# Performance work log

Measured on AMD Instinct MI355X. Metric: run time of the kernel, lower is better.

## Reference

```python
import jax, jax.numpy as jnp
import numpy as np

DIM_IN = 384
DIM_V = 384
NUM_HEADS = 8
DIM_FF = 1536
B, N = 4, 2048


def setup_inputs() -> dict:
    key = jax.random.key(0)
    ks = jax.random.split(key, 7)
    s_in = 1.0 / np.sqrt(DIM_IN)
    s_v = 1.0 / np.sqrt(DIM_V)
    s_ff = 1.0 / np.sqrt(DIM_FF)
    return {
        "x": jax.random.normal(ks[0], (B, N, DIM_IN), jnp.float32),
        "y": jax.random.normal(ks[1], (B, N, DIM_IN), jnp.float32),
        "Wq": jax.random.normal(ks[2], (DIM_V, DIM_IN), jnp.float32) * s_in,
        "Wk": jax.random.normal(ks[3], (DIM_V, DIM_IN), jnp.float32) * s_in,
        "Wv": jax.random.normal(ks[4], (DIM_V, DIM_IN), jnp.float32) * s_in,
        "W1": jax.random.normal(ks[5], (DIM_FF, DIM_V), jnp.float32) * s_v,
        "W2": jax.random.normal(ks[6], (DIM_V, DIM_FF), jnp.float32) * s_ff,
    }


def reference(x, y, Wq, Wk, Wv, W1, W2):
    H = NUM_HEADS
    d = DIM_V // H  # per-head dim
    Q = jnp.einsum('bnd,vd->bnv', x, Wq)
    K = jnp.einsum('bnd,vd->bnv', y, Wk)
    V = jnp.einsum('bnd,vd->bnv', y, Wv)
    # split channels into heads: [B, H, N, d]
    def to_heads(t):
        b, n, _ = t.shape
        return t.reshape(b, n, H, d).transpose(0, 2, 1, 3)
    Qh, Kh, Vh = to_heads(Q), to_heads(K), to_heads(V)
    # NOTE: original scales by sqrt(dim_V) (full model dim), not per-head dim
    scores = jnp.einsum('bhid,bhjd->bhij', Qh, Kh) / jnp.sqrt(jnp.float32(DIM_V))
    attn = jax.nn.softmax(scores, axis=-1)  # dropout = identity in eval
    A = jnp.einsum('bhij,bhjd->bhid', attn, Vh)
    # residual per-head, then merge heads back to [B, N, dim_V]
    O = (Qh + A).transpose(0, 2, 1, 3).reshape(x.shape[0], x.shape[1], DIM_V)
    # FFN with exact-erf gelu (torch F.gelu default) and residual
    hidden = jax.nn.gelu(jnp.einsum('bnv,fv->bnf', O, W1), approximate=False)
    O = O + jnp.einsum('bnf,vf->bnv', hidden, W2)
    return O
```

## Files before the change

kernel.cpp:

```cpp
#include <hip/hip_runtime.h>
#include <stdint.h>

#define NB 4
#define NSEQ 2048
#define DIN 384
#define DV 384
#define NH 8
#define DH 48
#define DFF 1536
#define MTOT (NB*NSEQ)
#define QBLK 128

typedef __attribute__((ext_vector_type(8))) short bf16x8;
typedef __attribute__((ext_vector_type(4))) float f32x4;
typedef unsigned short u16;

#define SCALE2 0.07362222f

__device__ __forceinline__ u16 f2bf(float f) {
  unsigned u = __builtin_bit_cast(unsigned, f);
  u = (u + 0x7FFFu + ((u >> 16) & 1u)) >> 16;
  return (u16)u;
}
__device__ __forceinline__ float bf2f(u16 h) {
  unsigned u = ((unsigned)h) << 16;
  return __builtin_bit_cast(float, u);
}
__device__ __forceinline__ float ex2(float x) {
  float r; asm("v_exp_f32 %0, %1" : "=v"(r) : "v"(x)); return r;
}
__device__ __forceinline__ float frcp(float x) {
  float r; asm("v_rcp_f32 %0, %1" : "=v"(r) : "v"(x)); return r;
}

__device__ __forceinline__ void gload16(const u16* g, u16* l) {
  __builtin_amdgcn_global_load_lds(
      (const __attribute__((address_space(1))) void*)g,
      (__attribute__((address_space(3))) void*)l, 16, 0, 0);
}

__global__ __launch_bounds__(256) void convert_k(
    const float* __restrict__ xf, const float* __restrict__ yf,
    const float* __restrict__ wq, const float* __restrict__ wk,
    const float* __restrict__ wv, const float* __restrict__ w1,
    const float* __restrict__ w2,
    u16* __restrict__ xb, u16* __restrict__ yb,
    u16* __restrict__ wqb, u16* __restrict__ wkb, u16* __restrict__ wvb,
    u16* __restrict__ w1b, u16* __restrict__ w2b) {
  long i = (long)blockIdx.x * 256 + threadIdx.x;
  const float* src; u16* dst; long u = i;
  if      (u < 786432)  { src = xf; dst = xb; }
  else if (u < 1572864) { u -= 786432;  src = yf; dst = yb; }
  else if (u < 1609728) { u -= 1572864; src = wq; dst = wqb; }
  else if (u < 1646592) { u -= 1609728; src = wk; dst = wkb; }
  else if (u < 1683456) { u -= 1646592; src = wv; dst = wvb; }
  else if (u < 1830912) { u -= 1683456; src = w1; dst = w1b; }
  else                  { u -= 1830912; src = w2; dst = w2b; }
  float4 v = ((const float4*)src)[u];
  ushort4 o;
  o.x = f2bf(v.x); o.y = f2bf(v.y); o.z = f2bf(v.z); o.w = f2bf(v.w);
  ((ushort4*)dst)[u] = o;
}

template<int EPI>
__device__ __forceinline__ void gemm_tile(const u16* __restrict__ A,
                                          const u16* __restrict__ Bw,
                                          int K, int ldk,
                                          int m0, int n0, int ldc,
                                          u16* __restrict__ Cb,
                                          float* __restrict__ Cf) {
  __shared__ __align__(16) u16 Al[128 * 64];
  __shared__ __align__(16) u16 Bl[128 * 64];
  const int t = threadIdx.x;
  const int l = t & 63, w = t >> 6;
  const int g = l >> 4, nn = l & 15;
  const int wm = w >> 1, wn = w & 1;
  f32x4 acc[4][4] = {};
  const int KT = K >> 6;
  for (int kt = 0; kt < KT; ++kt) {
    const int k0 = kt * 64;
    __syncthreads();
#pragma unroll
    for (int s = 0; s < 4; ++s) {
      int u = t + 256 * s; int r = u >> 3, ch = u & 7;
      int csw = (ch ^ (r & 7)) * 8;
      gload16(A  + (long)(m0 + r) * ldk + k0 + csw, Al + u * 8);
      gload16(Bw + (long)(n0 + r) * ldk + k0 + csw, Bl + u * 8);
    }
    __syncthreads();
#pragma unroll
    for (int ks = 0; ks < 2; ++ks) {
      const int slot = ((ks * 4 + g) ^ (nn & 7)) * 8;
      bf16x8 af[4], bfr[4];
#pragma unroll
      for (int mt = 0; mt < 4; ++mt)
        af[mt] = *(const bf16x8*)(Al + (wm * 64 + mt * 16 + nn) * 64 + slot);
#pragma unroll
      for (int nt = 0; nt < 4; ++nt)
        bfr[nt] = *(const bf16x8*)(Bl + (wn * 64 + nt * 16 + nn) * 64 + slot);
#pragma unroll
      for (int mt = 0; mt < 4; ++mt)
#pragma unroll
        for (int nt = 0; nt < 4; ++nt)
          acc[mt][nt] = __builtin_amdgcn_mfma_f32_16x16x32_bf16(af[mt], bfr[nt], acc[mt][nt], 0, 0, 0);
    }
  }
#pragma unroll
  for (int mt = 0; mt < 4; ++mt)
#pragma unroll
    for (int nt = 0; nt < 4; ++nt)
#pragma unroll
      for (int jr = 0; jr < 4; ++jr) {
        int gm = m0 + wm * 64 + mt * 16 + g * 4 + jr;
        int gn = n0 + wn * 64 + nt * 16 + nn;
        float v = acc[mt][nt][jr];
        if (EPI == 0) {
          Cb[(long)gm * ldc + gn] = f2bf(v);
        } else if (EPI == 1) {
          float inner = 0.7978845608f * v * (1.0f + 0.044715f * v * v);
          float tl = ex2(-2.885390082f * fabsf(inner));
          float th = (1.0f - tl) * frcp(1.0f + tl);
          th = copysignf(th, inner);
          Cb[(long)gm * ldc + gn] = f2bf(0.5f * v * (1.0f + th));
        } else if (EPI == 2) {
          unsafeAtomicAdd(&Cf[(long)gm * ldc + gn], v);
        } else {
          long vidx = ((long)(gm >> 11) * 384 + gn) * 2048 + (gm & 2047);
          Cb[vidx] = f2bf(v);
        }
      }
}

__global__ __launch_bounds__(256) void qkv_k(const u16* __restrict__ xb,
                                             const u16* __restrict__ yb,
                                             const u16* __restrict__ Wb,
                                             u16* __restrict__ QKVb) {
  int bx = blockIdx.x;
  int by = blockIdx.y;
  int mat = by / 3, ntile = by - mat * 3;
  const u16* A = (mat == 0) ? xb : yb;
  const u16* Bw = Wb + (long)mat * (DV * DIN);
  u16* C = QKVb + (long)mat * ((long)MTOT * DV);
  gemm_tile<0>(A, Bw, DIN, DIN, bx * 128, ntile * 128, DV, C, nullptr);
}

__global__ __launch_bounds__(256) void vt_k(const u16* __restrict__ yb,
                                            const u16* __restrict__ Wvb,
                                            u16* __restrict__ VT) {
  gemm_tile<3>(yb, Wvb, DIN, DIN, blockIdx.x * 128, blockIdx.y * 128, 0, VT, nullptr);
}

__global__ __launch_bounds__(256) void ffn1_k(const u16* __restrict__ Ob,
                                              const u16* __restrict__ W1b,
                                              u16* __restrict__ hid) {
  gemm_tile<1>(Ob, W1b, DV, DV, blockIdx.x * 128, blockIdx.y * 128, DFF, hid, nullptr);
}

__global__ __launch_bounds__(256) void ffn2_k(const u16* __restrict__ hid,
                                              const u16* __restrict__ W2b,
                                              float* __restrict__ Out) {
  int z = blockIdx.z;
  gemm_tile<2>(hid + z * 768, W2b + z * 768, 768, DFF,
               blockIdx.x * 128, blockIdx.y * 128, DV, nullptr, Out);
}

__global__ __launch_bounds__(512) void attn_k(const u16* __restrict__ Qb,
                                              const u16* __restrict__ Kb,
                                              const u16* __restrict__ VT,
                                              u16* __restrict__ Ob,
                                              float* __restrict__ Out) {
  __shared__ __align__(16) u16 Kl[2][128 * 64];
  __shared__ __align__(16) u16 Pl[128 * 128];

  int bx0 = blockIdx.x;
  int lg = (bx0 & 7) * 64 + (bx0 >> 3);
  int qt = lg & 15, h = (lg >> 4) & 7, b = lg >> 7;
  const int t = threadIdx.x, l = t & 63, w = t >> 6;
  const int g = l >> 4, n = l & 15;
  const long rowbase = (long)b * NSEQ;
  const int q0 = qt * QBLK;
  const int hc = h * DH;
  const u16* vt = VT + (long)(b * NH + h) * (DH * NSEQ);

  for (int i = t; i < 768; i += 512) {
    int r = i / 6, ch = i - r * 6;
    bf16x8 v = *(const bf16x8*)(Qb + (rowbase + q0 + r) * DV + hc + ch * 8);
    bf16x8 sv;
#pragma unroll
    for (int e = 0; e < 8; ++e) sv[e] = (short)f2bf(bf2f((u16)v[e]) * SCALE2);
    *(bf16x8*)(Pl + r * 64 + ch * 8) = sv;
  }
  if (t < 256) {
    int r = t >> 1;
    bf16x8 z = {};
    *(bf16x8*)(Pl + r * 64 + 48 + (t & 1) * 8) = z;
  }
#pragma unroll
  for (int s = 0; s < 2; ++s) {
    int u = t + 512 * s; int r = u >> 3, ch = u & 7;
    gload16(Kb + (rowbase + r) * DV + hc + ((ch ^ (r & 7)) * 8), &Kl[0][u * 8]);
  }
  __syncthreads();

  bf16x8 qa[2];
#pragma unroll
  for (int ks = 0; ks < 2; ++ks)
    qa[ks] = *(const bf16x8*)(Pl + (w * 16 + n) * 64 + ks * 32 + g * 8);

  float mL[4], sL[4];
#pragma unroll
  for (int jr = 0; jr < 4; ++jr) { mL[jr] = -1e30f; sL[jr] = 0.0f; }
  f32x4 oacc[3] = {};

  for (int c = 0; c < 16; ++c) {
    asm volatile("s_waitcnt vmcnt(0)" ::: "memory");
    __builtin_amdgcn_s_barrier();
    __builtin_amdgcn_sched_barrier(0);
    if (c + 1 < 16) {
      u16* dst = Kl[(c + 1) & 1];
#pragma unroll
      for (int s = 0; s < 2; ++s) {
        int u = t + 512 * s; int r = u >> 3, ch = u & 7;
        gload16(Kb + (rowbase + (c + 1) * 128 + r) * DV + hc + ((ch ^ (r & 7)) * 8),
                dst + u * 8);
      }
    }
    const u16* kbuf = Kl[c & 1];

    f32x4 sc[8];
#pragma unroll
    for (int jl = 0; jl < 8; ++jl) {
      f32x4 a = {};
#pragma unroll
      for (int ks = 0; ks < 2; ++ks) {
        bf16x8 kb2 = *(const bf16x8*)(kbuf + (jl * 16 + n) * 64 + (((ks * 4 + g) ^ (n & 7)) * 8));
        a = __builtin_amdgcn_mfma_f32_16x16x32_bf16(qa[ks], kb2, a, 0, 0, 0);
      }
      sc[jl] = a;
    }

#pragma unroll
    for (int jr = 0; jr < 4; ++jr) {
      float mx = fmaxf(fmaxf(fmaxf(sc[0][jr], sc[1][jr]), fmaxf(sc[2][jr], sc[3][jr])),
                       fmaxf(fmaxf(sc[4][jr], sc[5][jr]), fmaxf(sc[6][jr], sc[7][jr])));
      mx = fmaxf(mx, __shfl_xor(mx, 1, 64));
      mx = fmaxf(mx, __shfl_xor(mx, 2, 64));
      mx = fmaxf(mx, __shfl_xor(mx, 4, 64));
      mx = fmaxf(mx, __shfl_xor(mx, 8, 64));
      float mn = fmaxf(mL[jr], mx);
      float scl = ex2(mL[jr] - mn);
      mL[jr] = mn;
      float rs = 0.0f;
      u16* prl = Pl + (w * 16 + 4 * g + jr) * 128;
      const int pswz = ((4 * g + jr) & 7) << 3;
#pragma unroll
      for (int jl = 0; jl < 8; ++jl) {
        float p = ex2(sc[jl][jr] - mn);
        rs += p;
        prl[(jl * 16 + n) ^ pswz] = (u16)(__builtin_bit_cast(unsigned, p) >> 16);
      }
      rs += __shfl_xor(rs, 1, 64);
      rs += __shfl_xor(rs, 2, 64);
      rs += __shfl_xor(rs, 4, 64);
      rs += __shfl_xor(rs, 8, 64);
      sL[jr] = sL[jr] * scl + rs;
#pragma unroll
      for (int dt = 0; dt < 3; ++dt) oacc[dt][jr] *= scl;
    }

    const u16* vtc = vt + c * 128;
#pragma unroll
    for (int ks4 = 0; ks4 < 4; ++ks4) {
      bf16x8 pa = *(const bf16x8*)(Pl + (w * 16 + n) * 128 + ((ks4 * 32 + g * 8) ^ ((n & 7) * 8)));
#pragma unroll
      for (int dt = 0; dt < 3; ++dt) {
        bf16x8 vb = *(const bf16x8*)(vtc + (long)(dt * 16 + n) * NSEQ + ks4 * 32 + g * 8);
        oacc[dt] = __builtin_amdgcn_mfma_f32_16x16x32_bf16(pa, vb, oacc[dt], 0, 0, 0);
      }
    }
  }

#pragma unroll
  for (int jr = 0; jr < 4; ++jr) {
    float inv = 1.0f / sL[jr];
    long gr = rowbase + q0 + w * 16 + 4 * g + jr;
#pragma unroll
    for (int dt = 0; dt < 3; ++dt) {
      int col = hc + dt * 16 + n;
      float val = oacc[dt][jr] * inv;
      float q = bf2f(Qb[gr * DV + col]);
      float o = q + val;
      Out[gr * DV + col] = o;
      Ob[gr * DV + col] = f2bf(o);
    }
  }
}

extern "C" void kernel_launch(void* const* d_in, const int* in_sizes, int n_in,
                              void* d_out, int out_size, void* d_ws, size_t ws_size,
                              hipStream_t stream) {
  const float* xf = (const float*)d_in[0];
  const float* yf = (const float*)d_in[1];
  const float* wq = (const float*)d_in[2];
  const float* wk = (const float*)d_in[3];
  const float* wv = (const float*)d_in[4];
  const float* w1 = (const float*)d_in[5];
  const float* w2 = (const float*)d_in[6];
  float* Out = (float*)d_out;

  char* ws = (char*)d_ws;
  u16* xb   = (u16*)(ws + 0);
  u16* yb   = (u16*)(ws + 6291456);
  u16* QKVb = (u16*)(ws + 12582912);
  u16* Qb   = QKVb;
  u16* Kb   = (u16*)(ws + 18874368);
  u16* VT   = (u16*)(ws + 25165824);
  u16* Ob   = (u16*)(ws + 31457280);
  u16* Wqb  = (u16*)(ws + 37748736);
  u16* Wkb  = (u16*)(ws + 38043648);
  u16* Wvb  = (u16*)(ws + 38338560);
  u16* W1b  = (u16*)(ws + 38633472);
  u16* W2b  = (u16*)(ws + 39813120);
  u16* hid  = (u16*)(ws + 0);

  convert_k<<<7728, 256, 0, stream>>>(xf, yf, wq, wk, wv, w1, w2,
                                      xb, yb, Wqb, Wkb, Wvb, W1b, W2b);
  qkv_k<<<dim3(64, 6), 256, 0, stream>>>(xb, yb, Wqb, QKVb);
  vt_k<<<dim3(64, 3), 256, 0, stream>>>(yb, Wvb, VT);
  attn_k<<<512, 512, 0, stream>>>(Qb, Kb, VT, Ob, Out);
  ffn1_k<<<dim3(64, 12), 256, 0, stream>>>(Ob, W1b, hid);
  ffn2_k<<<dim3(64, 3, 2), 256, 0, stream>>>(hid, W2b, Out);
}
```

Before: 270.4 us.

## Fold V projection into QKV GEMM and transpose V in shared memory inside attention

Removes the separate vt_k launch that wrote a transposed V, and instead computes V row-major in the QKV GEMM by extending its grid to nine tiles. Inside attention, 192 threads prefetch the next V chunk into registers, transpose it into a swizzled LDS tile, and the PV MFMAs read from LDS instead of strided global memory. This saves a kernel launch and uncoalesced global V reads, at the cost of extra LDS, an added barrier per iteration, and more register pressure.

```diff
diff --git a/kernel.cpp b/kernel.cpp
--- a/kernel.cpp
+++ b/kernel.cpp
@@ -122,11 +122,8 @@
           float th = (1.0f - tl) * frcp(1.0f + tl);
           th = copysignf(th, inner);
           Cb[(long)gm * ldc + gn] = f2bf(0.5f * v * (1.0f + th));
-        } else if (EPI == 2) {
+        } else {
           unsafeAtomicAdd(&Cf[(long)gm * ldc + gn], v);
-        } else {
-          long vidx = ((long)(gm >> 11) * 384 + gn) * 2048 + (gm & 2047);
-          Cb[vidx] = f2bf(v);
         }
       }
 }
@@ -144,12 +141,6 @@
   gemm_tile<0>(A, Bw, DIN, DIN, bx * 128, ntile * 128, DV, C, nullptr);
 }
 
-__global__ __launch_bounds__(256) void vt_k(const u16* __restrict__ yb,
-                                            const u16* __restrict__ Wvb,
-                                            u16* __restrict__ VT) {
-  gemm_tile<3>(yb, Wvb, DIN, DIN, blockIdx.x * 128, blockIdx.y * 128, 0, VT, nullptr);
-}
-
 __global__ __launch_bounds__(256) void ffn1_k(const u16* __restrict__ Ob,
                                               const u16* __restrict__ W1b,
                                               u16* __restrict__ hid) {
@@ -166,10 +157,11 @@
 
 __global__ __launch_bounds__(512) void attn_k(const u16* __restrict__ Qb,
                                               const u16* __restrict__ Kb,
-                                              const u16* __restrict__ VT,
+                                              const u16* __restrict__ Vb,
                                               u16* __restrict__ Ob,
                                               float* __restrict__ Out) {
   __shared__ __align__(16) u16 Kl[2][128 * 64];
+  __shared__ __align__(16) u16 VTl[48 * 128];
   __shared__ __align__(16) u16 Pl[128 * 128];
 
   int bx0 = blockIdx.x;
@@ -180,7 +172,6 @@
   const long rowbase = (long)b * NSEQ;
   const int q0 = qt * QBLK;
   const int hc = h * DH;
-  const u16* vt = VT + (long)(b * NH + h) * (DH * NSEQ);
 
   for (int i = t; i < 768; i += 512) {
     int r = i / 6, ch = i - r * 6;
@@ -200,7 +191,20 @@
     int u = t + 512 * s; int r = u >> 3, ch = u & 7;
     gload16(Kb + (rowbase + r) * DV + hc + ((ch ^ (r & 7)) * 8), &Kl[0][u * 8]);
   }
-  __syncthreads();
+  bf16x8 v0, v1, v2, v3;
+  int vq = 0, vch = 0;
+  if (t >= 320) {
+    int j = t - 320;
+    vq = j & 31; vch = j >> 5;
+    const u16* vbase = Vb + (rowbase + 4 * vq) * DV + hc + vch * 8;
+    v0 = *(const bf16x8*)(vbase);
+    v1 = *(const bf16x8*)(vbase + DV);
+    v2 = *(const bf16x8*)(vbase + 2 * DV);
+    v3 = *(const bf16x8*)(vbase + 3 * DV);
+  }
+  asm volatile("s_waitcnt lgkmcnt(0)" ::: "memory");
+  __builtin_amdgcn_s_barrier();
+  __builtin_amdgcn_sched_barrier(0);
 
   bf16x8 qa[2];
 #pragma unroll
@@ -213,8 +217,16 @@
   f32x4 oacc[3] = {};
 
   for (int c = 0; c < 16; ++c) {
-    asm volatile("s_waitcnt vmcnt(0)" ::: "memory");
     __builtin_amdgcn_s_barrier();
+    __builtin_amdgcn_sched_barrier(0);
+    if (t >= 320) {
+#pragma unroll
+      for (int e = 0; e < 8; ++e) {
+        short4 pk; pk.x = v0[e]; pk.y = v1[e]; pk.z = v2[e]; pk.w = v3[e];
+        int d = vch * 8 + e;
+        *(short4*)(VTl + ((d * 128 + 4 * vq) ^ (e << 3))) = pk;
+      }
+    }
     __builtin_amdgcn_sched_barrier(0);
     if (c + 1 < 16) {
       u16* dst = Kl[(c + 1) & 1];
@@ -225,8 +237,22 @@
                 dst + u * 8);
       }
     }
+    __builtin_amdgcn_sched_barrier(0);
+    if (c < 15) { asm volatile("s_waitcnt vmcnt(2)" ::: "memory"); }
+    else        { asm volatile("s_waitcnt vmcnt(0)" ::: "memory"); }
+    asm volatile("s_waitcnt lgkmcnt(0)" ::: "memory");
+    __builtin_amdgcn_s_barrier();
+    __builtin_amdgcn_sched_barrier(0);
+
+    if (t >= 320 && c + 1 < 16) {
+      const u16* vbase = Vb + (rowbase + (c + 1) * 128 + 4 * vq) * DV + hc + vch * 8;
+      v0 = *(const bf16x8*)(vbase);
+      v1 = *(const bf16x8*)(vbase + DV);
+      v2 = *(const bf16x8*)(vbase + 2 * DV);
+      v3 = *(const bf16x8*)(vbase + 3 * DV);
+    }
+
     const u16* kbuf = Kl[c & 1];
-
     f32x4 sc[8];
 #pragma unroll
     for (int jl = 0; jl < 8; ++jl) {
@@ -268,13 +294,13 @@
       for (int dt = 0; dt < 3; ++dt) oacc[dt][jr] *= scl;
     }
 
-    const u16* vtc = vt + c * 128;
 #pragma unroll
     for (int ks4 = 0; ks4 < 4; ++ks4) {
-      bf16x8 pa = *(const bf16x8*)(Pl + (w * 16 + n) * 128 + ((ks4 * 32 + g * 8) ^ ((n & 7) * 8)));
+      const int slot = ((ks4 * 4 + g) ^ (n & 7)) * 8;
+      bf16x8 pa = *(const bf16x8*)(Pl + (w * 16 + n) * 128 + slot);
 #pragma unroll
       for (int dt = 0; dt < 3; ++dt) {
-        bf16x8 vb = *(const bf16x8*)(vtc + (long)(dt * 16 + n) * NSEQ + ks4 * 32 + g * 8);
+        bf16x8 vb = *(const bf16x8*)(VTl + (dt * 16 + n) * 128 + slot);
         oacc[dt] = __builtin_amdgcn_mfma_f32_16x16x32_bf16(pa, vb, oacc[dt], 0, 0, 0);
       }
     }
@@ -314,7 +340,7 @@
   u16* QKVb = (u16*)(ws + 12582912);
   u16* Qb   = QKVb;
   u16* Kb   = (u16*)(ws + 18874368);
-  u16* VT   = (u16*)(ws + 25165824);
+  u16* Vb   = (u16*)(ws + 25165824);
   u16* Ob   = (u16*)(ws + 31457280);
   u16* Wqb  = (u16*)(ws + 37748736);
   u16* Wkb  = (u16*)(ws + 38043648);
@@ -325,9 +351,8 @@
 
   convert_k<<<7728, 256, 0, stream>>>(xf, yf, wq, wk, wv, w1, w2,
                                       xb, yb, Wqb, Wkb, Wvb, W1b, W2b);
-  qkv_k<<<dim3(64, 6), 256, 0, stream>>>(xb, yb, Wqb, QKVb);
-  vt_k<<<dim3(64, 3), 256, 0, stream>>>(yb, Wvb, VT);
-  attn_k<<<512, 512, 0, stream>>>(Qb, Kb, VT, Ob, Out);
+  qkv_k<<<dim3(64, 9), 256, 0, stream>>>(xb, yb, Wqb, QKVb);
+  attn_k<<<512, 512, 0, stream>>>(Qb, Kb, Vb, Ob, Out);
   ffn1_k<<<dim3(64, 12), 256, 0, stream>>>(Ob, W1b, hid);
   ffn2_k<<<dim3(64, 3, 2), 256, 0, stream>>>(hid, W2b, Out);
 }
```

New measurement: 246.2 us. -8.9%, faster.
